# Kernel tuning notes

Measured on AMD Instinct MI355X. Metric: run time of the kernel, lower is better.

The kernel has to match this reference:

```python
import jax, jax.numpy as jnp
import numpy as np

N_NODES = 100000


def gcn_conv(x, W, b, src, dst, n_nodes):
    """PyG GCNConv: D^{-1/2} (A + I) D^{-1/2} X W + b (self loops added)."""
    xw = x @ W  # [N, F_out]
    # degree over A + I, counted on destination (col) side
    deg = jnp.zeros((n_nodes,), dtype=x.dtype).at[dst].add(1.0) + 1.0
    dinv = jax.lax.rsqrt(deg)  # deg >= 1, safe
    # edge messages with symmetric normalization
    coef = dinv[src] * dinv[dst]  # [E]
    msg = xw[src] * coef[:, None]  # [E, F_out]
    agg = jax.ops.segment_sum(msg, dst, num_segments=n_nodes)
    # self-loop contribution: dinv[i]^2 * xw[i]
    out = agg + xw * (dinv * dinv)[:, None]
    return out + b


def setup_inputs() -> dict:
    key = jax.random.key(0)
    k1, k2, k3, k4 = jax.random.split(key, 4)
    input_dim, hidden_dim, output_dim = 64, 64, 32
    n_edges = 1600000
    x = jax.random.normal(k1, (N_NODES, input_dim), dtype=jnp.float32)
    edge_index = jax.random.randint(k2, (2, n_edges), 0, N_NODES, dtype=jnp.int64)
    # Glorot-style init for GCN weights, zero bias (PyG default)
    s1 = (6.0 / (input_dim + hidden_dim)) ** 0.5
    s2 = (6.0 / (hidden_dim + output_dim)) ** 0.5
    W1 = jax.random.uniform(k3, (input_dim, hidden_dim), jnp.float32, -s1, s1)
    W2 = jax.random.uniform(k4, (hidden_dim, output_dim), jnp.float32, -s2, s2)
    b1 = jnp.zeros((hidden_dim,), jnp.float32)
    b2 = jnp.zeros((output_dim,), jnp.float32)
    return {"x": x, "edge_index": edge_index, "W1": W1, "b1": b1, "W2": W2, "b2": b2}


def reference(x, edge_index, W1, b1, W2, b2):
    src, dst = edge_index[0], edge_index[1]
    h = jax.nn.relu(gcn_conv(x, W1, b1, src, dst, N_NODES))
    return gcn_conv(h, W2, b2, src, dst, N_NODES)
```

## Files before the change

### kernel.cpp

```cpp
#include <hip/hip_runtime.h>
#include <hip/hip_fp16.h>

#define NPB   64
#define KMAX  1600
#define BCAP  1408
#define CCAP  1920
#define EPB   8192

typedef _Float16 f16x8 __attribute__((ext_vector_type(8)));
typedef float    f32x4 __attribute__((ext_vector_type(4)));

__global__ __launch_bounds__(256) void bucket_scatter(
    const int* __restrict__ src, const int* __restrict__ dst, int E, int K,
    int* __restrict__ bucket_fill, unsigned* __restrict__ bucket_edges) {
    __shared__ int hist[KMAX];
    __shared__ int lbase[KMAX];
    __shared__ int gbase[KMAX];
    __shared__ unsigned sorted[EPB];
    __shared__ unsigned short bid[EPB];
    __shared__ int wsum[4];
    const int t = threadIdx.x;
    for (int i = t; i < K; i += 256) hist[i] = 0;
    __syncthreads();
    const int e0 = blockIdx.x * EPB;
    const int m = min(EPB, E - e0);
    for (int e = t; e < m; e += 256) atomicAdd(&hist[dst[e0 + e] >> 6], 1);
    __syncthreads();
    constexpr int CH = (KMAX + 255) / 256;
    int c[CH]; int s = 0;
#pragma unroll
    for (int j = 0; j < CH; ++j) { int idx = t * CH + j; c[j] = (idx < K) ? hist[idx] : 0; s += c[j]; }
    int lane = t & 63, w = t >> 6;
    int x = s;
    for (int d = 1; d < 64; d <<= 1) { int y = __shfl_up(x, d, 64); if (lane >= d) x += y; }
    if (lane == 63) wsum[w] = x;
    __syncthreads();
    int run = x - s;
    for (int j = 0; j < 4; ++j) if (j < w) run += wsum[j];
#pragma unroll
    for (int j = 0; j < CH; ++j) {
        int idx = t * CH + j;
        if (idx < K) {
            lbase[idx] = run;
            if (c[j] > 0) gbase[idx] = atomicAdd(&bucket_fill[idx], c[j]);
            run += c[j];
        }
    }
    __syncthreads();
    for (int i = t; i < K; i += 256) hist[i] = 0;
    __syncthreads();
    for (int e = t; e < m; e += 256) {
        int d = dst[e0 + e], b = d >> 6;
        int r = atomicAdd(&hist[b], 1);
        int pos = lbase[b] + r;
        sorted[pos] = ((unsigned)(d & 63) << 17) | (unsigned)src[e0 + e];
        bid[pos] = (unsigned short)b;
    }
    __syncthreads();
    for (int i = t; i < m; i += 256) {
        int b = bid[i];
        int off = gbase[b] + (i - lbase[b]);
        if (off < BCAP) bucket_edges[(size_t)b * BCAP + off] = sorted[i];
    }
}

__global__ __launch_bounds__(256) void bucket_csr(
    const int* __restrict__ bucket_fill, const unsigned* __restrict__ bucket_edges,
    unsigned* __restrict__ csr, int* __restrict__ rowstart, int* __restrict__ deg,
    float* __restrict__ dinv, int N, unsigned PAD) {
    __shared__ unsigned list[BCAP];
    __shared__ int cnt[NPB], pref[NPB], cnt2[NPB];
    const int b = blockIdx.x;
    const int m = min(bucket_fill[b], BCAP);
    if (threadIdx.x < NPB) { cnt[threadIdx.x] = 0; cnt2[threadIdx.x] = 0; }
    __syncthreads();
    const unsigned* bep = bucket_edges + (size_t)b * BCAP;
    for (int e = threadIdx.x; e < m; e += 256) {
        unsigned pk = bep[e];
        list[e] = pk;
        atomicAdd(&cnt[pk >> 17], 1);
    }
    __syncthreads();
    if (threadIdx.x < 64) {
        int lane = threadIdx.x;
        int c = cnt[lane];
        int cpad = (c + 7) & ~7;
        int x = cpad;
        for (int d = 1; d < 64; d <<= 1) {
            int y = __shfl_up(x, d, 64);
            if (lane >= d) x += y;
        }
        int ex = x - cpad;
        pref[lane] = ex;
        int g = b * NPB + lane;
        if (g < N) {
            deg[g] = c;
            rowstart[g] = b * CCAP + ex;
            dinv[g] = rsqrtf((float)c + 1.0f);
        }
        for (int p = c; p < cpad; ++p) {
            int ci = ex + p;
            if (ci < CCAP) csr[(size_t)b * CCAP + ci] = PAD;
        }
    }
    __syncthreads();
    for (int e = threadIdx.x; e < m; e += 256) {
        unsigned pk = list[e];
        int dl = pk >> 17;
        int r = atomicAdd(&cnt2[dl], 1);
        int ci = pref[dl] + r;
        if (ci < CCAP) csr[(size_t)b * CCAP + ci] = pk & 0x1FFFF;
    }
}

__global__ void wtrans_k(const float* __restrict__ W1, const float* __restrict__ W2,
                         __half* __restrict__ W1T, __half* __restrict__ W2T) {
    int t = threadIdx.x;
    for (int i = t; i < 64 * 64; i += 256) {
        int f = i >> 6, k = i & 63;
        W1T[i] = __float2half(W1[k * 64 + f]);
    }
    for (int i = t; i < 32 * 64; i += 256) {
        int f = i >> 6, k = i & 63;
        W2T[i] = __float2half(W2[k * 32 + f]);
    }
}

__global__ __launch_bounds__(256) void gemm1_mfma(
    const float* __restrict__ X, const __half* __restrict__ W1T,
    const float* __restrict__ dinv, __half* __restrict__ out, int N) {
    const int wave = threadIdx.x >> 6, lane = threadIdx.x & 63;
    const int r = lane & 15, q = lane >> 4;
    const int nb = blockIdx.x * 16;
    const int node = nb + r;
    const int col = wave * 16 + r;
    f32x4 acc = {0.f, 0.f, 0.f, 0.f};
#pragma unroll
    for (int kt = 0; kt < 2; ++kt) {
        const float4* xr = (const float4*)(X + (size_t)node * 64 + kt * 32 + q * 8);
        float4 p0 = xr[0], p1 = xr[1];
        f16x8 a;
        a[0] = (_Float16)p0.x; a[1] = (_Float16)p0.y; a[2] = (_Float16)p0.z; a[3] = (_Float16)p0.w;
        a[4] = (_Float16)p1.x; a[5] = (_Float16)p1.y; a[6] = (_Float16)p1.z; a[7] = (_Float16)p1.w;
        f16x8 b = *(const f16x8*)(W1T + (size_t)col * 64 + kt * 32 + q * 8);
        acc = __builtin_amdgcn_mfma_f32_16x16x32_f16(a, b, acc, 0, 0, 0);
    }
#pragma unroll
    for (int i = 0; i < 4; ++i) {
        int nd = nb + q * 4 + i;
        out[(size_t)nd * 64 + wave * 16 + r] = __float2half(acc[i] * dinv[nd]);
    }
}

__global__ __launch_bounds__(256) void gemm2_mfma(
    const __half* __restrict__ H, const __half* __restrict__ W2T,
    const float* __restrict__ dinv, __half* __restrict__ out, int N) {
    const int wave = threadIdx.x >> 6, lane = threadIdx.x & 63;
    const int r = lane & 15, q = lane >> 4;
    const int nb = blockIdx.x * 32 + (wave >> 1) * 16;
    const int cb = (wave & 1) * 16;
    const int node = nb + r;
    const int col = cb + r;
    f32x4 acc = {0.f, 0.f, 0.f, 0.f};
#pragma unroll
    for (int kt = 0; kt < 2; ++kt) {
        f16x8 a = *(const f16x8*)(H + (size_t)node * 64 + kt * 32 + q * 8);
        f16x8 b = *(const f16x8*)(W2T + (size_t)col * 64 + kt * 32 + q * 8);
        acc = __builtin_amdgcn_mfma_f32_16x16x32_f16(a, b, acc, 0, 0, 0);
    }
#pragma unroll
    for (int i = 0; i < 4; ++i) {
        int nd = nb + q * 4 + i;
        out[(size_t)nd * 32 + cb + r] = __float2half(acc[i] * dinv[nd]);
    }
}

template <int F, bool RELU, typename OT>
__global__ __launch_bounds__(256) void aggregate_h2(
    const __half* __restrict__ xws, const unsigned* __restrict__ csr,
    const int* __restrict__ rowstart, const int* __restrict__ deg,
    const float* __restrict__ dinv, const float* __restrict__ bias,
    OT* __restrict__ out, int n) {
    constexpr int LPN = F / 2;
    int t = blockIdx.x * 256 + threadIdx.x;
    int node = t / LPN;
    int fl = t % LPN;
    if (node >= n) return;
    int mp = (deg[node] + 7) & ~7;
    const unsigned* cp = csr + rowstart[node];
    const __half2* tab = (const __half2*)xws;
    float2 acc = __half22float2(tab[(size_t)node * LPN + fl]);
    for (int e = 0; e < mp; e += 8) {
        unsigned s0 = cp[e+0], s1 = cp[e+1], s2 = cp[e+2], s3 = cp[e+3];
        unsigned s4 = cp[e+4], s5 = cp[e+5], s6 = cp[e+6], s7 = cp[e+7];
        float2 a0 = __half22float2(tab[(size_t)s0 * LPN + fl]);
        float2 a1 = __half22float2(tab[(size_t)s1 * LPN + fl]);
        float2 a2 = __half22float2(tab[(size_t)s2 * LPN + fl]);
        float2 a3 = __half22float2(tab[(size_t)s3 * LPN + fl]);
        float2 a4 = __half22float2(tab[(size_t)s4 * LPN + fl]);
        float2 a5 = __half22float2(tab[(size_t)s5 * LPN + fl]);
        float2 a6 = __half22float2(tab[(size_t)s6 * LPN + fl]);
        float2 a7 = __half22float2(tab[(size_t)s7 * LPN + fl]);
        acc.x += ((a0.x + a1.x) + (a2.x + a3.x)) + ((a4.x + a5.x) + (a6.x + a7.x));
        acc.y += ((a0.y + a1.y) + (a2.y + a3.y)) + ((a4.y + a5.y) + (a6.y + a7.y));
    }
    float dn = dinv[node];
    float2 bf = ((const float2*)bias)[fl];
    float vx = acc.x * dn + bf.x;
    float vy = acc.y * dn + bf.y;
    if (RELU) { vx = fmaxf(vx, 0.f); vy = fmaxf(vy, 0.f); }
    if constexpr (sizeof(OT) == 4) {
        ((__half2*)out)[(size_t)node * LPN + fl] = __floats2half2_rn(vx, vy);
    } else {
        ((float2*)out)[(size_t)node * LPN + fl] = make_float2(vx, vy);
    }
}


extern "C" void kernel_launch(void* const* d_in, const int* in_sizes, int n_in,
                              void* d_out, int out_size, void* d_ws, size_t ws_size,
                              hipStream_t stream) {
    const float* x  = (const float*)d_in[0];
    const int*   ei = (const int*)d_in[1];
    const float* W1 = (const float*)d_in[2];
    const float* b1 = (const float*)d_in[3];
    const float* W2 = (const float*)d_in[4];
    const float* b2 = (const float*)d_in[5];
    float* out = (float*)d_out;

    const int N = in_sizes[0] / 64;
    const int E = in_sizes[1] / 2;
    const int K = (N + NPB - 1) / NPB;
    const int* src = ei;
    const int* dst = ei + E;

    unsigned* be    = (unsigned*)d_ws;
    unsigned* csr   = be + (size_t)K * BCAP;
    int*      bfill = (int*)(csr + (size_t)K * CCAP);
    int*      rowst = bfill + K;
    int*      deg   = rowst + N;
    float*    dinv  = (float*)(deg + N);
    __half*   xws   = (__half*)(dinv + N);
    __half*   h     = xws + (size_t)(N + 1) * 64;
    __half*   hw2   = h + (size_t)N * 64;
    __half*   W1T   = hw2 + (size_t)(N + 1) * 32;
    __half*   W2T   = W1T + 64 * 64;

    hipMemsetAsync(bfill, 0, (size_t)K * sizeof(int), stream);
    hipMemsetAsync(xws + (size_t)N * 64, 0, 64 * sizeof(__half), stream);
    hipMemsetAsync(hw2 + (size_t)N * 32, 0, 32 * sizeof(__half), stream);

    int sb = (E + EPB - 1) / EPB;
    bucket_scatter<<<sb, 256, 0, stream>>>(src, dst, E, K, bfill, be);
    wtrans_k<<<1, 256, 0, stream>>>(W1, W2, W1T, W2T);
    bucket_csr<<<K, 256, 0, stream>>>(bfill, be, csr, rowst, deg, dinv, N, (unsigned)N);

    gemm1_mfma<<<N / 16, 256, 0, stream>>>(x, W1T, dinv, xws, N);
    aggregate_h2<64, true, __half2><<<(N * 32 + 255) / 256, 256, 0, stream>>>(
        xws, csr, rowst, deg, dinv, b1, (__half2*)h, N);
    gemm2_mfma<<<N / 32, 256, 0, stream>>>(h, W2T, dinv, hw2, N);
    aggregate_h2<32, false, float2><<<(N * 16 + 255) / 256, 256, 0, stream>>>(
        hw2, csr, rowst, deg, dinv, b2, (float2*)out, N);
}
```

Baseline: 266.7 us.

## Simplify bucket scatter to direct atomics and widen aggregation to 16-byte loads

The bucket scatter kernel drops its shared-memory local sort and block-wide prefix scan. It now reserves global slots per bucket with one atomic and writes each edge directly, using smaller edge blocks (2048) so more blocks run at once. The aggregation kernels switch from 4-byte half2 gathers per lane to 16-byte (8 halves) gathers per lane, which cuts lane count and the number of load instructions per neighbor row. The trade-off is scattered global writes in the scatter kernel and fewer threads per node, so less parallelism, in aggregation.

```diff
diff --git a/kernel.cpp b/kernel.cpp
--- a/kernel.cpp
+++ b/kernel.cpp
@@ -5,7 +5,7 @@
 #define KMAX  1600
 #define BCAP  1408
 #define CCAP  1920
-#define EPB   8192
+#define EPB   2048
 
 typedef _Float16 f16x8 __attribute__((ext_vector_type(8)));
 typedef float    f32x4 __attribute__((ext_vector_type(4)));
@@ -14,53 +14,27 @@
     const int* __restrict__ src, const int* __restrict__ dst, int E, int K,
     int* __restrict__ bucket_fill, unsigned* __restrict__ bucket_edges) {
     __shared__ int hist[KMAX];
-    __shared__ int lbase[KMAX];
-    __shared__ int gbase[KMAX];
-    __shared__ unsigned sorted[EPB];
-    __shared__ unsigned short bid[EPB];
-    __shared__ int wsum[4];
+    __shared__ int base[KMAX];
     const int t = threadIdx.x;
     for (int i = t; i < K; i += 256) hist[i] = 0;
     __syncthreads();
     const int e0 = blockIdx.x * EPB;
-    const int m = min(EPB, E - e0);
-    for (int e = t; e < m; e += 256) atomicAdd(&hist[dst[e0 + e] >> 6], 1);
-    __syncthreads();
-    constexpr int CH = (KMAX + 255) / 256;
-    int c[CH]; int s = 0;
-#pragma unroll
-    for (int j = 0; j < CH; ++j) { int idx = t * CH + j; c[j] = (idx < K) ? hist[idx] : 0; s += c[j]; }
-    int lane = t & 63, w = t >> 6;
-    int x = s;
-    for (int d = 1; d < 64; d <<= 1) { int y = __shfl_up(x, d, 64); if (lane >= d) x += y; }
-    if (lane == 63) wsum[w] = x;
-    __syncthreads();
-    int run = x - s;
-    for (int j = 0; j < 4; ++j) if (j < w) run += wsum[j];
-#pragma unroll
-    for (int j = 0; j < CH; ++j) {
-        int idx = t * CH + j;
-        if (idx < K) {
-            lbase[idx] = run;
-            if (c[j] > 0) gbase[idx] = atomicAdd(&bucket_fill[idx], c[j]);
-            run += c[j];
-        }
-    }
-    __syncthreads();
-    for (int i = t; i < K; i += 256) hist[i] = 0;
-    __syncthreads();
-    for (int e = t; e < m; e += 256) {
-        int d = dst[e0 + e], b = d >> 6;
-        int r = atomicAdd(&hist[b], 1);
-        int pos = lbase[b] + r;
-        sorted[pos] = ((unsigned)(d & 63) << 17) | (unsigned)src[e0 + e];
-        bid[pos] = (unsigned short)b;
-    }
-    __syncthreads();
-    for (int i = t; i < m; i += 256) {
-        int b = bid[i];
-        int off = gbase[b] + (i - lbase[b]);
-        if (off < BCAP) bucket_edges[(size_t)b * BCAP + off] = sorted[i];
+    const int e1 = min(e0 + EPB, E);
+    for (int e = e0 + t; e < e1; e += 256)
+        atomicAdd(&hist[dst[e] >> 6], 1);
+    __syncthreads();
+    for (int b = t; b < K; b += 256) {
+        int h = hist[b];
+        base[b] = h ? atomicAdd(&bucket_fill[b], h) : 0;
+    }
+    __syncthreads();
+    for (int e = e0 + t; e < e1; e += 256) {
+        int d = dst[e];
+        int bb = d >> 6;
+        int pos = atomicAdd(&base[bb], 1);
+        if (pos < BCAP)
+            bucket_edges[(size_t)bb * BCAP + pos] =
+                ((unsigned)(d & 63) << 17) | (unsigned)src[e];
     }
 }
 
@@ -175,44 +149,64 @@
     }
 }
 
-template <int F, bool RELU, typename OT>
-__global__ __launch_bounds__(256) void aggregate_h2(
+template <int F, bool RELU, bool HOUT>
+__global__ __launch_bounds__(256) void aggregate_w(
     const __half* __restrict__ xws, const unsigned* __restrict__ csr,
     const int* __restrict__ rowstart, const int* __restrict__ deg,
     const float* __restrict__ dinv, const float* __restrict__ bias,
-    OT* __restrict__ out, int n) {
-    constexpr int LPN = F / 2;
+    void* __restrict__ outv, int n) {
+    constexpr int LPN = F / 8;
     int t = blockIdx.x * 256 + threadIdx.x;
     int node = t / LPN;
-    int fl = t % LPN;
+    int fl = t - node * LPN;
     if (node >= n) return;
     int mp = (deg[node] + 7) & ~7;
     const unsigned* cp = csr + rowstart[node];
-    const __half2* tab = (const __half2*)xws;
-    float2 acc = __half22float2(tab[(size_t)node * LPN + fl]);
+    const float4* tab = (const float4*)xws;
+    float4 sv = tab[(size_t)node * LPN + fl];
+    float acc[8];
+    {
+        const __half2* sh = (const __half2*)&sv;
+#pragma unroll
+        for (int j = 0; j < 4; ++j) { float2 v = __half22float2(sh[j]); acc[2*j] = v.x; acc[2*j+1] = v.y; }
+    }
     for (int e = 0; e < mp; e += 8) {
-        unsigned s0 = cp[e+0], s1 = cp[e+1], s2 = cp[e+2], s3 = cp[e+3];
-        unsigned s4 = cp[e+4], s5 = cp[e+5], s6 = cp[e+6], s7 = cp[e+7];
-        float2 a0 = __half22float2(tab[(size_t)s0 * LPN + fl]);
-        float2 a1 = __half22float2(tab[(size_t)s1 * LPN + fl]);
-        float2 a2 = __half22float2(tab[(size_t)s2 * LPN + fl]);
-        float2 a3 = __half22float2(tab[(size_t)s3 * LPN + fl]);
-        float2 a4 = __half22float2(tab[(size_t)s4 * LPN + fl]);
-        float2 a5 = __half22float2(tab[(size_t)s5 * LPN + fl]);
-        float2 a6 = __half22float2(tab[(size_t)s6 * LPN + fl]);
-        float2 a7 = __half22float2(tab[(size_t)s7 * LPN + fl]);
-        acc.x += ((a0.x + a1.x) + (a2.x + a3.x)) + ((a4.x + a5.x) + (a6.x + a7.x));
-        acc.y += ((a0.y + a1.y) + (a2.y + a3.y)) + ((a4.y + a5.y) + (a6.y + a7.y));
+        unsigned s[8];
+#pragma unroll
+        for (int u = 0; u < 8; ++u) s[u] = cp[e + u];
+        float4 d[8];
+#pragma unroll
+        for (int u = 0; u < 8; ++u) d[u] = tab[(size_t)s[u] * LPN + fl];
+#pragma unroll
+        for (int u = 0; u < 8; ++u) {
+            const __half2* dh = (const __half2*)&d[u];
+#pragma unroll
+            for (int j = 0; j < 4; ++j) {
+                float2 v = __half22float2(dh[j]);
+                acc[2*j] += v.x; acc[2*j+1] += v.y;
+            }
+        }
     }
     float dn = dinv[node];
-    float2 bf = ((const float2*)bias)[fl];
-    float vx = acc.x * dn + bf.x;
-    float vy = acc.y * dn + bf.y;
-    if (RELU) { vx = fmaxf(vx, 0.f); vy = fmaxf(vy, 0.f); }
-    if constexpr (sizeof(OT) == 4) {
-        ((__half2*)out)[(size_t)node * LPN + fl] = __floats2half2_rn(vx, vy);
+    float4 b0 = ((const float4*)bias)[fl * 2];
+    float4 b1 = ((const float4*)bias)[fl * 2 + 1];
+    float bf[8] = {b0.x, b0.y, b0.z, b0.w, b1.x, b1.y, b1.z, b1.w};
+    float v[8];
+#pragma unroll
+    for (int j = 0; j < 8; ++j) {
+        v[j] = acc[j] * dn + bf[j];
+        if (RELU) v[j] = fmaxf(v[j], 0.f);
+    }
+    if constexpr (HOUT) {
+        __half2 o[4];
+#pragma unroll
+        for (int j = 0; j < 4; ++j) o[j] = __floats2half2_rn(v[2*j], v[2*j+1]);
+        ((float4*)outv)[(size_t)node * LPN + fl] = *(const float4*)o;
     } else {
-        ((float2*)out)[(size_t)node * LPN + fl] = make_float2(vx, vy);
+        float4 o0 = {v[0], v[1], v[2], v[3]};
+        float4 o1 = {v[4], v[5], v[6], v[7]};
+        float4* op = (float4*)outv + ((size_t)node * F + fl * 8) / 4;
+        op[0] = o0; op[1] = o1;
     }
 }
 
@@ -256,9 +250,9 @@
     bucket_csr<<<K, 256, 0, stream>>>(bfill, be, csr, rowst, deg, dinv, N, (unsigned)N);
 
     gemm1_mfma<<<N / 16, 256, 0, stream>>>(x, W1T, dinv, xws, N);
-    aggregate_h2<64, true, __half2><<<(N * 32 + 255) / 256, 256, 0, stream>>>(
-        xws, csr, rowst, deg, dinv, b1, (__half2*)h, N);
+    aggregate_w<64, true, true><<<(N * 8 + 255) / 256, 256, 0, stream>>>(
+        xws, csr, rowst, deg, dinv, b1, h, N);
     gemm2_mfma<<<N / 32, 256, 0, stream>>>(h, W2T, dinv, hw2, N);
-    aggregate_h2<32, false, float2><<<(N * 16 + 255) / 256, 256, 0, stream>>>(
-        hw2, csr, rowst, deg, dinv, b2, (float2*)out, N);
-}
+    aggregate_w<32, false, false><<<(N * 4 + 255) / 256, 256, 0, stream>>>(
+        hw2, csr, rowst, deg, dinv, b2, out, N);
+}
```

New measurement: 264.1 us. No clear change (-1.0%).
